# Kernel tuning notes

Hardware: AMD Instinct MI355X
Metric: run time of the kernel (lower is better)

The kernel has to match this reference:

```python
import jax, jax.numpy as jnp
import numpy as np

N, D = 8192, 256
TEMPERATURE = 1.0
K_NEIGHBORS = 5  # min(5, N-1)
EPS = 1e-08


def setup_inputs() -> dict:
    key = jax.random.key(0)
    k1, k2 = jax.random.split(key)
    node_embeddings = jax.random.normal(k1, (N, D), dtype=jnp.float32)
    adj_matrix = jax.random.uniform(k2, (N, N), dtype=jnp.float32)
    return {"node_embeddings": node_embeddings, "adj_matrix": adj_matrix}


def _components(node_embeddings, adj_matrix):
    n = node_embeddings.shape[0]

    # --- total energy ---
    kinetic = jnp.sum(node_embeddings ** 2, axis=-1)  # [N]
    neighbor_emb = adj_matrix @ node_embeddings       # [N, D]
    potential = -jnp.sum(node_embeddings * neighbor_emb, axis=-1)
    degrees = jnp.sum(adj_matrix, axis=-1)
    total_energy = kinetic + potential / (degrees + EPS)

    # --- local entropy (cosine sims masked by adjacency, softmax rowwise) ---
    norms = jnp.linalg.norm(node_embeddings, axis=-1, keepdims=True)
    normalized = node_embeddings / jnp.maximum(norms, 1e-12)  # F.normalize eps
    similarities = normalized @ normalized.T                  # [N, N]
    masked = similarities * adj_matrix
    row_sums = jnp.sum(adj_matrix, axis=1)
    probs = jax.nn.softmax(masked / TEMPERATURE, axis=1)
    ent = -jnp.sum(probs * jnp.log(probs + EPS), axis=1)
    local_entropy = jnp.where(row_sums > 0, ent, 0.0)

    # --- equilibrium deviation (global + KNN-local) ---
    global_mean = jnp.mean(node_embeddings, axis=0, keepdims=True)
    global_dev = jnp.linalg.norm(node_embeddings - global_mean, axis=-1)
    sq = jnp.sum(node_embeddings ** 2, axis=-1)
    d2 = sq[:, None] + sq[None, :] - 2.0 * (node_embeddings @ node_embeddings.T)
    dist = jnp.sqrt(jnp.maximum(d2, 0.0))  # torch.cdist equivalent
    _, topk_idx = jax.lax.top_k(-dist, K_NEIGHBORS + 1)  # smallest k+1
    neighbor_idx = topk_idx[:, 1:]                        # drop self, [N, K]
    local_means = jnp.mean(node_embeddings[neighbor_idx], axis=1)  # [N, D]
    local_dev = jnp.linalg.norm(node_embeddings - local_means, axis=-1)
    equilibrium_deviation = 0.6 * global_dev + 0.4 * local_dev

    # --- structural centrality ---
    degree_centrality = degrees / (n - 1 + EPS)
    emb_norms = jnp.linalg.norm(node_embeddings, axis=-1)
    emb_centrality = emb_norms / (jnp.max(emb_norms) + EPS)
    structural_centrality = 0.5 * degree_centrality + 0.5 * emb_centrality

    return jnp.stack([total_energy, local_entropy, equilibrium_deviation, structural_centrality])  # [4, N]


def reference(node_embeddings, adj_matrix):
    return _components(node_embeddings, adj_matrix)
```

## Files before the change

kernel.cpp:

```cpp
#include <hip/hip_runtime.h>
#include <math.h>

#define N 8192
#define D 256
#define EPSF 1e-8f
#define NJS 2
#define ROWS 32
#define JSPAN 4096
#define NCH 32

#define WS_SQ    0
#define WS_RINV  (N)
#define WS_GMEAN (2*N)
#define WS_MAXN  (2*N+256)
#define WS_COLP  (2*N+512)
#define WS_P0    (2*N+512+65536)
#define WS_EBF   (WS_P0+56*N)

typedef __attribute__((ext_vector_type(8))) short bf16x8;
typedef __attribute__((ext_vector_type(4))) float f32x4;

__device__ __forceinline__ unsigned short f2bf(float f) {
    unsigned u = __float_as_uint(f);
    u += 0x7fffu + ((u >> 16) & 1u);
    return (unsigned short)(u >> 16);
}

#if __has_builtin(__builtin_amdgcn_fmed3f)
#define MED3(a,b,c) __builtin_amdgcn_fmed3f((a),(b),(c))
#else
#define MED3(a,b,c) fmaxf(fminf((a),(b)), fminf(fmaxf((a),(b)),(c)))
#endif

#define PINS6(T, x) do {                                                        \
    float _x = (x);                                                             \
    float _n0 = fminf((T)[0], _x);                                              \
    float _n1 = MED3((T)[0], (T)[1], _x);                                       \
    float _n2 = MED3((T)[1], (T)[2], _x);                                       \
    float _n3 = MED3((T)[2], (T)[3], _x);                                       \
    float _n4 = MED3((T)[3], (T)[4], _x);                                       \
    float _n5 = MED3((T)[4], (T)[5], _x);                                       \
    (T)[0]=_n0; (T)[1]=_n1; (T)[2]=_n2; (T)[3]=_n3; (T)[4]=_n4; (T)[5]=_n5;     \
  } while (0)

__global__ void k_prep(const float* __restrict__ emb, float* __restrict__ ws,
                       unsigned short* __restrict__ ebf) {
    if (blockIdx.x < 2048) {
        int row = blockIdx.x * 4 + (threadIdx.x >> 6);
        int lane = threadIdx.x & 63;
        float4 v = *(const float4*)(emb + (size_t)row * D + lane * 4);
        ushort4 b;
        b.x = f2bf(v.x); b.y = f2bf(v.y); b.z = f2bf(v.z); b.w = f2bf(v.w);
        *(ushort4*)(ebf + (size_t)row * D + lane * 4) = b;
        float s = v.x * v.x + v.y * v.y + v.z * v.z + v.w * v.w;
#pragma unroll
        for (int mk = 32; mk >= 1; mk >>= 1) s += __shfl_xor(s, mk);
        if (lane == 0) {
            ws[WS_SQ + row] = s;
            ws[WS_RINV + row] = 1.0f / fmaxf(sqrtf(s), 1e-12f);
        }
    } else {
        int d = threadIdx.x;
        int b = blockIdx.x - 2048;
        float s = 0.f;
        for (int r = b * 32; r < b * 32 + 32; ++r) s += emb[(size_t)r * D + d];
        ws[WS_COLP + b * 256 + d] = s;
    }
}

__global__ void k_colred(float* __restrict__ ws) {
    __shared__ float red[256];
    int d = threadIdx.x;
    float s = 0.f;
    for (int b = 0; b < 256; ++b) s += ws[WS_COLP + b * 256 + d];
    ws[WS_GMEAN + d] = s * (1.0f / N);
    float mx = 0.f;
    for (int i = d; i < N; i += 256) mx = fmaxf(mx, ws[WS_SQ + i]);
    red[d] = mx;
    __syncthreads();
#pragma unroll
    for (int st2 = 128; st2 >= 1; st2 >>= 1) {
        if (d < st2) red[d] = fmaxf(red[d], red[d + st2]);
        __syncthreads();
    }
    if (d == 0) ws[WS_MAXN] = sqrtf(red[0]);
}

#define STAGE(PTR, SOFF, K0) do {                                               \
    _Pragma("unroll")                                                           \
    for (int q = 0; q < 4; ++q) {                                               \
      __builtin_amdgcn_global_load_lds(                                         \
        (const __attribute__((address_space(1))) void*)(ebf + gbase + (SOFF) + (K0) + q * (8 * D)), \
        (__attribute__((address_space(3))) void*)&(PTR)[((w << 5) + (q << 3)) * 64], \
        16, 0, 0);                                                              \
    } } while (0)

#define VMW(NLIT) do {                                                          \
    asm volatile("s_waitcnt vmcnt(" #NLIT ")" ::: "memory");                    \
    __builtin_amdgcn_sched_barrier(0);                                          \
  } while (0)

#define SBAR() __builtin_amdgcn_sched_barrier(0)

#define COMP(PTR, H) do {                                                       \
    _Pragma("unroll")                                                           \
    for (int ksl = 0; ksl < 2; ++ksl) {                                         \
      const int pg = ((ksl << 2) + g) ^ (lid & 7);                              \
      bf16x8 afr[2];                                                            \
      _Pragma("unroll")                                                         \
      for (int mf = 0; mf < 2; ++mf)                                            \
        afr[mf] = *(const bf16x8*)&(PTR)[((w << 5) + (mf << 4) + lid) * 64 + (pg << 3)]; \
      _Pragma("unroll")                                                         \
      for (int nf = 0; nf < 2; ++nf)                                            \
        _Pragma("unroll")                                                       \
        for (int mf = 0; mf < 2; ++mf)                                          \
          acc[nf][mf] = __builtin_amdgcn_mfma_f32_16x16x32_bf16(                \
              afr[mf], bfr[nf][(H) * 2 + ksl], acc[nf][mf], 0, 0, 0);           \
    } } while (0)

__global__ __launch_bounds__(256) void k_main(
    const float* __restrict__ adj,
    const unsigned short* __restrict__ ebf,
    const float* __restrict__ ws,
    float* __restrict__ pout)
{
    __shared__ unsigned short tile0[128 * 64];
    __shared__ unsigned short tile1[128 * 64];
    __shared__ unsigned short tile2[128 * 64];
    __shared__ unsigned short tile3[128 * 64];

    const int tid = threadIdx.x;
    const int w = tid >> 6;
    const int l = tid & 63;
    const int lid = l & 15;
    const int g = l >> 4;
    const int srow = l >> 3;
    const int sc = (l & 7) ^ srow;
    const int panel = blockIdx.x >> 1;
    const int js = blockIdx.x & 1;
    const int row0 = panel * ROWS;
    const int j0 = js * JSPAN;

    const float* sq = ws + WS_SQ;
    const float* rinv = ws + WS_RINV;
    const size_t gbase = (size_t)(j0 + (w << 5) + srow) * D + (sc << 3);

    bf16x8 bfr[2][8];
    float rvr[2];
    int r_[2];
#pragma unroll
    for (int nf = 0; nf < 2; ++nf) {
        int r = row0 + nf * 16 + lid;
        r_[nf] = r;
        rvr[nf] = rinv[r];
#pragma unroll
        for (int ks = 0; ks < 8; ++ks)
            bfr[nf][ks] = *(const bf16x8*)(ebf + (size_t)r * D + ks * 32 + g * 8);
    }

    float deg[2] = {0.f, 0.f}, pot[2] = {0.f, 0.f};
    float sl[2] = {0.f, 0.f}, st[2] = {0.f, 0.f};
    float tv[2][6];
#pragma unroll
    for (int nf = 0; nf < 2; ++nf)
#pragma unroll
        for (int s2 = 0; s2 < 6; ++s2) tv[nf][s2] = 1e30f;

    f32x4 acc[2][2];
#pragma unroll
    for (int nf = 0; nf < 2; ++nf)
#pragma unroll
        for (int mf = 0; mf < 2; ++mf) acc[nf][mf] = (f32x4){0.f, 0.f, 0.f, 0.f};
    f32x4 advA[2][2], sqv[2], rvv[2];

    STAGE(tile0, 0, 0);
    STAGE(tile1, 0, 64);
    STAGE(tile2, 0, 128);
    STAGE(tile3, 0, 192);

#pragma unroll 1
    for (int cc = 0; cc < NCH; ++cc) {
        const int jj = j0 + cc * 128 + (w << 5);
        const size_t snext = (size_t)(cc + 1) * (128 * D);

#pragma unroll
        for (int nf = 0; nf < 2; ++nf)
#pragma unroll
            for (int mf = 0; mf < 2; ++mf)
                advA[nf][mf] = __builtin_nontemporal_load(
                    (const f32x4*)(adj + (size_t)r_[nf] * N + jj + mf * 16 + g * 4));
        VMW(16);
        COMP(tile0, 0);
        SBAR();
        STAGE(tile0, snext, 0);

#pragma unroll
        for (int mf = 0; mf < 2; ++mf) {
            sqv[mf] = *(const f32x4*)(sq + jj + mf * 16 + g * 4);
            rvv[mf] = *(const f32x4*)(rinv + jj + mf * 16 + g * 4);
        }
        VMW(20);
        COMP(tile1, 1);
        SBAR();
        STAGE(tile1, snext, 64);

        VMW(16);
        COMP(tile2, 2);
        SBAR();
        STAGE(tile2, snext, 128);

        VMW(8);
        COMP(tile3, 3);
        SBAR();
        STAGE(tile3, snext, 192);
#pragma unroll
        for (int nf = 0; nf < 2; ++nf) {
#pragma unroll
            for (int mf = 0; mf < 2; ++mf) {
#pragma unroll
                for (int e = 0; e < 4; ++e) {
                    const float gv = acc[nf][mf][e];
                    const float a = advA[nf][mf][e];
                    const int j = jj + mf * 16 + g * 4 + e;
                    deg[nf] += a;
                    pot[nf] = fmaf(a, gv, pot[nf]);
                    const float s = (gv * rvr[nf]) * (rvv[mf][e] * a);
                    const float ex = __expf(s);
                    sl[nf] += ex;
                    st[nf] = fmaf(ex, s, st[nf]);
                    const float dp = fmaf(-2.f, gv, sqv[mf][e]);
                    const float key = __uint_as_float(
                        (__float_as_uint(dp) & 0xFFFFE000u) | (unsigned)j);
                    PINS6(tv[nf], key);
                }
                acc[nf][mf] = (f32x4){0.f, 0.f, 0.f, 0.f};
            }
        }
    }

#pragma unroll
    for (int nf = 0; nf < 2; ++nf) {
#pragma unroll
        for (int mk = 16; mk <= 32; mk <<= 1) {
            deg[nf] += __shfl_xor(deg[nf], mk);
            pot[nf] += __shfl_xor(pot[nf], mk);
            sl[nf] += __shfl_xor(sl[nf], mk);
            st[nf] += __shfl_xor(st[nf], mk);
            float ok[6];
#pragma unroll
            for (int s2 = 0; s2 < 6; ++s2) ok[s2] = __shfl_xor(tv[nf][s2], mk);
#pragma unroll
            for (int s2 = 0; s2 < 6; ++s2) PINS6(tv[nf], ok[s2]);
        }
    }

    __syncthreads();
    float* lds_s = (float*)&tile0[0];
    float* lds_k = lds_s + 4 * 32 * 4;
#pragma unroll
    for (int nf = 0; nf < 2; ++nf) {
        if (g == 0) {
            int lr = nf * 16 + lid;
            lds_s[(w * 32 + lr) * 4 + 0] = deg[nf];
            lds_s[(w * 32 + lr) * 4 + 1] = pot[nf];
            lds_s[(w * 32 + lr) * 4 + 2] = sl[nf];
            lds_s[(w * 32 + lr) * 4 + 3] = st[nf];
#pragma unroll
            for (int s2 = 0; s2 < 6; ++s2)
                lds_k[(w * 32 + lr) * 6 + s2] = tv[nf][s2];
        }
    }
    __syncthreads();

    if (tid < 32) {
        float dg = 0.f, pt = 0.f, ll = 0.f, tt = 0.f;
#pragma unroll
        for (int w2 = 0; w2 < 4; ++w2) {
            dg += lds_s[(w2 * 32 + tid) * 4 + 0];
            pt += lds_s[(w2 * 32 + tid) * 4 + 1];
            ll += lds_s[(w2 * 32 + tid) * 4 + 2];
            tt += lds_s[(w2 * 32 + tid) * 4 + 3];
        }
        float mk6[6];
#pragma unroll
        for (int s2 = 0; s2 < 6; ++s2) mk6[s2] = lds_k[tid * 6 + s2];
#pragma unroll
        for (int w2 = 1; w2 < 4; ++w2)
#pragma unroll
            for (int s2 = 0; s2 < 6; ++s2)
                PINS6(mk6, lds_k[(w2 * 32 + tid) * 6 + s2]);
        const int slot = js * N + row0 + tid;
        pout[slot] = dg;
        pout[2 * N + slot] = pt;
        pout[4 * N + slot] = ll;
        pout[6 * N + slot] = tt;
#pragma unroll
        for (int s2 = 0; s2 < 6; ++s2)
            pout[8 * N + slot * 6 + s2] = mk6[s2];
    }
}

__global__ void k_final(const float* __restrict__ emb, const float* __restrict__ ws,
                        float* __restrict__ out) {
    int row = blockIdx.x * 4 + (threadIdx.x >> 6);
    int lane = threadIdx.x & 63;
    const float* p0 = ws + WS_P0;

    float dg = 0.f, pt = 0.f, ll = 0.f, tt = 0.f;
#pragma unroll
    for (int js = 0; js < NJS; ++js) {
        int slot = js * N + row;
        dg += p0[slot]; pt += p0[2 * N + slot];
        ll += p0[4 * N + slot]; tt += p0[6 * N + slot];
    }

    float keys[6];
#pragma unroll
    for (int s = 0; s < 6; ++s) keys[s] = p0[8 * N + (size_t)row * 6 + s];
#pragma unroll
    for (int s = 0; s < 6; ++s) PINS6(keys, p0[8 * N + (size_t)(N + row) * 6 + s]);
    int nb[5];
#pragma unroll
    for (int t = 0; t < 5; ++t) nb[t] = (int)(__float_as_uint(keys[t + 1]) & 0x1FFFu);

    float4 e = *(const float4*)(emb + (size_t)row * D + lane * 4);
    float4 gm = *(const float4*)(ws + WS_GMEAN + lane * 4);
    float gx = e.x - gm.x, gy = e.y - gm.y, gz = e.z - gm.z, gw = e.w - gm.w;
    float gd = gx * gx + gy * gy + gz * gz + gw * gw;
    float ax = 0.f, ay = 0.f, az = 0.f, aw = 0.f;
#pragma unroll
    for (int t = 0; t < 5; ++t) {
        float4 nv = *(const float4*)(emb + (size_t)nb[t] * D + lane * 4);
        ax += nv.x; ay += nv.y; az += nv.z; aw += nv.w;
    }
    ax *= 0.2f; ay *= 0.2f; az *= 0.2f; aw *= 0.2f;
    float lx = e.x - ax, ly = e.y - ay, lz = e.z - az, lw = e.w - aw;
    float ld = lx * lx + ly * ly + lz * lz + lw * lw;
#pragma unroll
    for (int mk = 32; mk >= 1; mk >>= 1) {
        gd += __shfl_xor(gd, mk);
        ld += __shfl_xor(ld, mk);
    }
    if (lane == 0) {
        float sqv = ws[WS_SQ + row];
        float mn = ws[WS_MAXN];
        float ent = logf(ll) - tt / ll;
        out[row] = sqv - pt / (dg + EPSF);
        out[N + row] = (dg > 0.f) ? ent : 0.f;
        out[2 * N + row] = 0.6f * sqrtf(gd) + 0.4f * sqrtf(ld);
        out[3 * N + row] = 0.5f * (dg / (8191.0f + EPSF)) + 0.5f * (sqrtf(sqv) / (mn + EPSF));
    }
}

extern "C" void kernel_launch(void* const* d_in, const int* in_sizes, int n_in,
                              void* d_out, int out_size, void* d_ws, size_t ws_size,
                              hipStream_t stream) {
    const float* emb = (const float*)d_in[0];
    const float* adj = (const float*)d_in[1];
    float* out = (float*)d_out;
    float* ws = (float*)d_ws;
    unsigned short* ebf = (unsigned short*)(ws + WS_EBF);

    k_prep<<<2304, 256, 0, stream>>>(emb, ws, ebf);
    k_colred<<<1, 256, 0, stream>>>(ws);
    k_main<<<512, 256, 0, stream>>>(adj, ebf, ws, ws + WS_P0);
    k_final<<<N / 4, 256, 0, stream>>>(emb, ws, out);
}
```

Before: 159.5 us.

## Split main kernel into single-wave blocks over eight column spans, use exp2

Restructures k_main from 512 four-wave blocks to 2048 single-wave blocks, each covering 1024 columns instead of 4096. The cross-wave LDS reduction and its barriers go away, and each wave writes its partials straight to global memory. k_final now merges eight partial sets instead of two. It also folds log2(e) into the row scale so the exponent can use the hardware exp2, rescaling the entropy term at the end, and zeroes the accumulators through the MFMA C operand instead of with separate resets. This gains occupancy and drops block synchronisation, at the cost of more partial-result traffic and less LDS tile sharing per block.

```diff
diff --git a/kernel.cpp b/kernel.cpp
--- a/kernel.cpp
+++ b/kernel.cpp
@@ -4,9 +4,9 @@
 #define N 8192
 #define D 256
 #define EPSF 1e-8f
-#define NJS 2
+#define NJS 8
 #define ROWS 32
-#define JSPAN 4096
+#define JSPAN 1024
 #define NCH 32
 
 #define WS_SQ    0
@@ -15,7 +15,7 @@
 #define WS_MAXN  (2*N+256)
 #define WS_COLP  (2*N+512)
 #define WS_P0    (2*N+512+65536)
-#define WS_EBF   (WS_P0+56*N)
+#define WS_EBF   (WS_P0+80*N)
 
 typedef __attribute__((ext_vector_type(8))) short bf16x8;
 typedef __attribute__((ext_vector_type(4))) float f32x4;
@@ -25,6 +25,12 @@
     u += 0x7fffu + ((u >> 16) & 1u);
     return (unsigned short)(u >> 16);
 }
+
+#if __has_builtin(__builtin_amdgcn_exp2f)
+#define EXP2(x) __builtin_amdgcn_exp2f(x)
+#else
+#define EXP2(x) exp2f(x)
+#endif
 
 #if __has_builtin(__builtin_amdgcn_fmed3f)
 #define MED3(a,b,c) __builtin_amdgcn_fmed3f((a),(b),(c))
@@ -91,7 +97,7 @@
     for (int q = 0; q < 4; ++q) {                                               \
       __builtin_amdgcn_global_load_lds(                                         \
         (const __attribute__((address_space(1))) void*)(ebf + gbase + (SOFF) + (K0) + q * (8 * D)), \
-        (__attribute__((address_space(3))) void*)&(PTR)[((w << 5) + (q << 3)) * 64], \
+        (__attribute__((address_space(3))) void*)&(PTR)[(q << 3) * 64],         \
         16, 0, 0);                                                              \
     } } while (0)
 
@@ -109,50 +115,50 @@
       bf16x8 afr[2];                                                            \
       _Pragma("unroll")                                                         \
       for (int mf = 0; mf < 2; ++mf)                                            \
-        afr[mf] = *(const bf16x8*)&(PTR)[((w << 5) + (mf << 4) + lid) * 64 + (pg << 3)]; \
+        afr[mf] = *(const bf16x8*)&(PTR)[((mf << 4) + lid) * 64 + (pg << 3)];   \
       _Pragma("unroll")                                                         \
       for (int nf = 0; nf < 2; ++nf)                                            \
         _Pragma("unroll")                                                       \
         for (int mf = 0; mf < 2; ++mf)                                          \
           acc[nf][mf] = __builtin_amdgcn_mfma_f32_16x16x32_bf16(                \
-              afr[mf], bfr[nf][(H) * 2 + ksl], acc[nf][mf], 0, 0, 0);           \
+              afr[mf], bfr[nf][(H) * 2 + ksl],                                  \
+              ((H) == 0 && ksl == 0) ? z4 : acc[nf][mf], 0, 0, 0);              \
     } } while (0)
 
-__global__ __launch_bounds__(256) void k_main(
+__global__ __launch_bounds__(64) void k_main(
     const float* __restrict__ adj,
     const unsigned short* __restrict__ ebf,
     const float* __restrict__ ws,
     float* __restrict__ pout)
 {
-    __shared__ unsigned short tile0[128 * 64];
-    __shared__ unsigned short tile1[128 * 64];
-    __shared__ unsigned short tile2[128 * 64];
-    __shared__ unsigned short tile3[128 * 64];
-
-    const int tid = threadIdx.x;
-    const int w = tid >> 6;
-    const int l = tid & 63;
+    __shared__ unsigned short tile0[32 * 64];
+    __shared__ unsigned short tile1[32 * 64];
+    __shared__ unsigned short tile2[32 * 64];
+    __shared__ unsigned short tile3[32 * 64];
+
+    const int l = threadIdx.x;
     const int lid = l & 15;
     const int g = l >> 4;
     const int srow = l >> 3;
     const int sc = (l & 7) ^ srow;
-    const int panel = blockIdx.x >> 1;
-    const int js = blockIdx.x & 1;
+    const int panel = blockIdx.x >> 3;
+    const int js = blockIdx.x & 7;
     const int row0 = panel * ROWS;
     const int j0 = js * JSPAN;
 
     const float* sq = ws + WS_SQ;
     const float* rinv = ws + WS_RINV;
-    const size_t gbase = (size_t)(j0 + (w << 5) + srow) * D + (sc << 3);
+    const size_t gbase = (size_t)(j0 + srow) * D + (sc << 3);
+    const f32x4 z4 = (f32x4){0.f, 0.f, 0.f, 0.f};
 
     bf16x8 bfr[2][8];
-    float rvr[2];
+    float rvr2[2];
     int r_[2];
 #pragma unroll
     for (int nf = 0; nf < 2; ++nf) {
         int r = row0 + nf * 16 + lid;
         r_[nf] = r;
-        rvr[nf] = rinv[r];
+        rvr2[nf] = rinv[r] * 1.44269504f;
 #pragma unroll
         for (int ks = 0; ks < 8; ++ks)
             bfr[nf][ks] = *(const bf16x8*)(ebf + (size_t)r * D + ks * 32 + g * 8);
@@ -170,7 +176,7 @@
 #pragma unroll
     for (int nf = 0; nf < 2; ++nf)
 #pragma unroll
-        for (int mf = 0; mf < 2; ++mf) acc[nf][mf] = (f32x4){0.f, 0.f, 0.f, 0.f};
+        for (int mf = 0; mf < 2; ++mf) acc[nf][mf] = z4;
     f32x4 advA[2][2], sqv[2], rvv[2];
 
     STAGE(tile0, 0, 0);
@@ -180,8 +186,8 @@
 
 #pragma unroll 1
     for (int cc = 0; cc < NCH; ++cc) {
-        const int jj = j0 + cc * 128 + (w << 5);
-        const size_t snext = (size_t)(cc + 1) * (128 * D);
+        const int jj = j0 + cc * 32;
+        const size_t snext = (size_t)(cc + 1) * (32 * D);
 
 #pragma unroll
         for (int nf = 0; nf < 2; ++nf)
@@ -224,16 +230,15 @@
                     const int j = jj + mf * 16 + g * 4 + e;
                     deg[nf] += a;
                     pot[nf] = fmaf(a, gv, pot[nf]);
-                    const float s = (gv * rvr[nf]) * (rvv[mf][e] * a);
-                    const float ex = __expf(s);
+                    const float s2v = (gv * rvr2[nf]) * (rvv[mf][e] * a);
+                    const float ex = EXP2(s2v);
                     sl[nf] += ex;
-                    st[nf] = fmaf(ex, s, st[nf]);
+                    st[nf] = fmaf(ex, s2v, st[nf]);
                     const float dp = fmaf(-2.f, gv, sqv[mf][e]);
                     const float key = __uint_as_float(
                         (__float_as_uint(dp) & 0xFFFFE000u) | (unsigned)j);
                     PINS6(tv[nf], key);
                 }
-                acc[nf][mf] = (f32x4){0.f, 0.f, 0.f, 0.f};
             }
         }
     }
@@ -252,51 +257,16 @@
 #pragma unroll
             for (int s2 = 0; s2 < 6; ++s2) PINS6(tv[nf], ok[s2]);
         }
-    }
-
-    __syncthreads();
-    float* lds_s = (float*)&tile0[0];
-    float* lds_k = lds_s + 4 * 32 * 4;
-#pragma unroll
-    for (int nf = 0; nf < 2; ++nf) {
         if (g == 0) {
-            int lr = nf * 16 + lid;
-            lds_s[(w * 32 + lr) * 4 + 0] = deg[nf];
-            lds_s[(w * 32 + lr) * 4 + 1] = pot[nf];
-            lds_s[(w * 32 + lr) * 4 + 2] = sl[nf];
-            lds_s[(w * 32 + lr) * 4 + 3] = st[nf];
+            const int slot = js * N + row0 + nf * 16 + lid;
+            pout[slot] = deg[nf];
+            pout[8 * N + slot] = pot[nf];
+            pout[16 * N + slot] = sl[nf];
+            pout[24 * N + slot] = st[nf];
 #pragma unroll
             for (int s2 = 0; s2 < 6; ++s2)
-                lds_k[(w * 32 + lr) * 6 + s2] = tv[nf][s2];
-        }
-    }
-    __syncthreads();
-
-    if (tid < 32) {
-        float dg = 0.f, pt = 0.f, ll = 0.f, tt = 0.f;
-#pragma unroll
-        for (int w2 = 0; w2 < 4; ++w2) {
-            dg += lds_s[(w2 * 32 + tid) * 4 + 0];
-            pt += lds_s[(w2 * 32 + tid) * 4 + 1];
-            ll += lds_s[(w2 * 32 + tid) * 4 + 2];
-            tt += lds_s[(w2 * 32 + tid) * 4 + 3];
-        }
-        float mk6[6];
-#pragma unroll
-        for (int s2 = 0; s2 < 6; ++s2) mk6[s2] = lds_k[tid * 6 + s2];
-#pragma unroll
-        for (int w2 = 1; w2 < 4; ++w2)
-#pragma unroll
-            for (int s2 = 0; s2 < 6; ++s2)
-                PINS6(mk6, lds_k[(w2 * 32 + tid) * 6 + s2]);
-        const int slot = js * N + row0 + tid;
-        pout[slot] = dg;
-        pout[2 * N + slot] = pt;
-        pout[4 * N + slot] = ll;
-        pout[6 * N + slot] = tt;
-#pragma unroll
-        for (int s2 = 0; s2 < 6; ++s2)
-            pout[8 * N + slot * 6 + s2] = mk6[s2];
+                pout[32 * N + (size_t)slot * 6 + s2] = tv[nf][s2];
+        }
     }
 }
 
@@ -310,15 +280,18 @@
 #pragma unroll
     for (int js = 0; js < NJS; ++js) {
         int slot = js * N + row;
-        dg += p0[slot]; pt += p0[2 * N + slot];
-        ll += p0[4 * N + slot]; tt += p0[6 * N + slot];
+        dg += p0[slot]; pt += p0[8 * N + slot];
+        ll += p0[16 * N + slot]; tt += p0[24 * N + slot];
     }
 
     float keys[6];
 #pragma unroll
-    for (int s = 0; s < 6; ++s) keys[s] = p0[8 * N + (size_t)row * 6 + s];
-#pragma unroll
-    for (int s = 0; s < 6; ++s) PINS6(keys, p0[8 * N + (size_t)(N + row) * 6 + s]);
+    for (int s = 0; s < 6; ++s) keys[s] = p0[32 * N + (size_t)row * 6 + s];
+#pragma unroll
+    for (int js = 1; js < NJS; ++js)
+#pragma unroll
+        for (int s = 0; s < 6; ++s)
+            PINS6(keys, p0[32 * N + (size_t)(js * N + row) * 6 + s]);
     int nb[5];
 #pragma unroll
     for (int t = 0; t < 5; ++t) nb[t] = (int)(__float_as_uint(keys[t + 1]) & 0x1FFFu);
@@ -344,7 +317,7 @@
     if (lane == 0) {
         float sqv = ws[WS_SQ + row];
         float mn = ws[WS_MAXN];
-        float ent = logf(ll) - tt / ll;
+        float ent = logf(ll) - (tt * 0.6931471805599453f) / ll;
         out[row] = sqv - pt / (dg + EPSF);
         out[N + row] = (dg > 0.f) ? ent : 0.f;
         out[2 * N + row] = 0.6f * sqrtf(gd) + 0.4f * sqrtf(ld);
@@ -363,6 +336,6 @@
 
     k_prep<<<2304, 256, 0, stream>>>(emb, ws, ebf);
     k_colred<<<1, 256, 0, stream>>>(ws);
-    k_main<<<512, 256, 0, stream>>>(adj, ebf, ws, ws + WS_P0);
+    k_main<<<2048, 64, 0, stream>>>(adj, ebf, ws, ws + WS_P0);
     k_final<<<N / 4, 256, 0, stream>>>(emb, ws, out);
 }
```

Measured after the change: 162.8 us. 2.0% more time.
